# Performance work log

Measured on AMD Instinct MI355X. Metric: run time of the kernel, lower is better.

Reference implementation:

```python
import jax, jax.numpy as jnp
import numpy as np

N = 2048            # num nodes
AVG_DEG = 16
E0 = N * AVG_DEG    # random edges; self-loops appended -> E = E0 + N
IN_FEATS = 256
H = 16              # num_heads
HS = 32             # hidden_size (forced by linear001 = Linear(32,16))
D = HS // H         # head_dim = 2
EPS = 1e-5


def gat_conv(x, src, dst, W, al, ar, b):
    # DGL-style GATConv: x [N,F] -> [N,H,D]
    feat = (x @ W).reshape(N, H, D)                      # [N,H,D]
    el = (feat * al[None]).sum(-1)                       # [N,H] (src term)
    er = (feat * ar[None]).sum(-1)                       # [N,H] (dst term)
    e = jax.nn.leaky_relu(el[src] + er[dst], 0.2)        # [E,H]
    m = jax.ops.segment_max(e, dst, num_segments=N)      # segment softmax over incoming edges
    ex = jnp.exp(e - m[dst])
    s = jax.ops.segment_sum(ex, dst, num_segments=N)
    alpha = ex / s[dst]                                  # [E,H]
    out = jax.ops.segment_sum(alpha[:, :, None] * feat[src], dst, num_segments=N)
    return out + b.reshape(1, H, D)


def setup_inputs() -> dict:
    key = jax.random.key(0)
    ks = jax.random.split(key, 40)
    rn = lambda k, s, sc=0.1: (jax.random.normal(k, s, jnp.float32) * sc)
    loops = jnp.arange(N, dtype=jnp.int32)
    src = jnp.concatenate([jax.random.randint(ks[0], (E0,), 0, N, jnp.int32), loops])
    dst = jnp.concatenate([jax.random.randint(ks[1], (E0,), 0, N, jnp.int32), loops])
    inp = {
        'features': jax.random.normal(ks[2], (N, IN_FEATS), jnp.float32),
        'src': src, 'dst': dst,
        # GATConv 1
        'W1': rn(ks[3], (IN_FEATS, HS)), 'al1': rn(ks[4], (H, D)), 'ar1': rn(ks[5], (H, D)), 'bg1': rn(ks[6], (HS,)),
        # GATConv 2
        'W2': rn(ks[7], (HS, HS)), 'al2': rn(ks[8], (H, D)), 'ar2': rn(ks[9], (H, D)), 'bg2': rn(ks[10], (HS,)),
        # dense MHA projections
        'qw': rn(ks[11], (HS, HS)), 'qb': rn(ks[12], (HS,)),
        'kw': rn(ks[13], (HS, HS)), 'kb': rn(ks[14], (HS,)),
        'vw': rn(ks[15], (HS, HS)), 'vb': rn(ks[16], (HS,)),
        'ow': rn(ks[17], (HS, HS)), 'ob': rn(ks[18], (HS,)),
        # batchnorm affine
        'bn_g': jnp.ones((HS,), jnp.float32), 'bn_b': jnp.zeros((HS,), jnp.float32),
        # mlp
        'm1w': rn(ks[19], (HS, HS // 2)), 'm1b': rn(ks[20], (HS // 2,)),
        'm2w': rn(ks[21], (HS // 2, HS)), 'm2b': rn(ks[22], (HS,)),
        # scoring head
        'w001': rn(ks[23], (32, 16)), 'b001': rn(ks[24], (16,)),
        'w01': rn(ks[25], (16, 8)), 'b01': rn(ks[26], (8,)),
        'w1': rn(ks[27], (8, 4)), 'b1': rn(ks[28], (4,)),
        'w2': rn(ks[29], (4, 1)), 'b2': rn(ks[30], (1,)),
    }
    return inp


def reference(features, src, dst, W1, al1, ar1, bg1, W2, al2, ar2, bg2,
              qw, qb, kw, kb, vw, vb, ow, ob, bn_g, bn_b,
              m1w, m1b, m2w, m2b, w001, b001, w01, b01, w1, b1, w2, b2):
    h = gat_conv(features, src, dst, W1, al1, ar1, bg1).reshape(N, HS)
    h = gat_conv(h, src, dst, W2, al2, ar2, bg2).reshape(N, HS)
    # manual dense multi-head attention across all nodes
    Q = (h @ qw + qb).reshape(N, H, D)
    K = (h @ kw + kb).reshape(N, H, D)
    V = (h @ vw + vb).reshape(N, H, D)
    scores = jnp.einsum('nhd,mhd->hnm', Q, K) / jnp.sqrt(jnp.float32(D))  # [H,N,N]
    attn = jax.nn.softmax(scores, axis=-1)
    ao = jnp.einsum('hnm,mhd->nhd', attn, V).reshape(N, HS)
    ao = ao @ ow + ob
    # BatchNorm1d (training mode: batch stats, biased variance)
    mu = ao.mean(0)
    var = ao.var(0)
    ao = (ao - mu) / jnp.sqrt(var + EPS) * bn_g + bn_b
    # MLP
    ao = jax.nn.relu(ao @ m1w + m1b)
    ao = jax.nn.relu(ao @ m2w + m2b)
    # scoring head
    z = jax.nn.leaky_relu(ao @ w001 + b001, 0.01)
    z = jax.nn.leaky_relu(z @ w01 + b01, 0.01)
    z = jax.nn.leaky_relu(z @ w1 + b1, 0.01)
    return jax.nn.sigmoid(z @ w2 + b2)  # [N,1]
```

## Files before the change

### kernel.cpp

```cpp
#include <hip/hip_runtime.h>
#include <math.h>

#define NN 2048
#define NH 16
#define HSZ 32
#define INF_ 256

__global__ void k_gat1(const float* __restrict__ x, const float* __restrict__ W,
                       const float* __restrict__ al, const float* __restrict__ ar,
                       float* __restrict__ feat, float* __restrict__ el,
                       float* __restrict__ er, int* __restrict__ cnt,
                       int* __restrict__ cur, float* __restrict__ bnbuf) {
    __shared__ float xs[INF_];
    __shared__ float ps[256];
    __shared__ float fs[HSZ];
    int n = blockIdx.x, tid = threadIdx.x;
    xs[tid] = x[(size_t)n * INF_ + tid];
    if (tid == 0) cnt[n] = 0;
    if (tid == 1) cur[n] = 0;
    if (n == 0 && tid >= 128 && tid < 192) bnbuf[tid - 128] = 0.f;
    __syncthreads();
    int j = tid & 31, part = tid >> 5;
    float a = 0.f;
#pragma unroll
    for (int kk = 0; kk < 32; ++kk) {
        int k = part * 32 + kk;
        a += xs[k] * W[k * HSZ + j];
    }
    ps[tid] = a;
    __syncthreads();
    if (tid < HSZ) {
        float s = 0.f;
#pragma unroll
        for (int p = 0; p < 8; ++p) s += ps[p * 32 + tid];
        fs[tid] = s;
        feat[n * HSZ + tid] = s;
    }
    __syncthreads();
    if (tid < NH) {
        el[n * NH + tid] = fs[2 * tid] * al[2 * tid] + fs[2 * tid + 1] * al[2 * tid + 1];
    } else if (tid < 2 * NH) {
        int hh = tid - NH;
        er[n * NH + hh] = fs[2 * hh] * ar[2 * hh] + fs[2 * hh + 1] * ar[2 * hh + 1];
    }
}

__global__ void k_hist(int E, const int* __restrict__ dst, int* __restrict__ cnt) {
    int i = blockIdx.x * 256 + threadIdx.x;
    if (i < E) atomicAdd(&cnt[dst[i]], 1);
}

__global__ void k_scan(const int* __restrict__ cnt, int* __restrict__ off, int E) {
    __shared__ int ps[256];
    int t = threadIdx.x;
    int base = t * 8;
    int loc[8];
    int s = 0;
#pragma unroll
    for (int j = 0; j < 8; ++j) {
        loc[j] = s;
        s += cnt[base + j];
    }
    ps[t] = s;
    __syncthreads();
    for (int st = 1; st < 256; st <<= 1) {
        int v = (t >= st) ? ps[t - st] : 0;
        __syncthreads();
        ps[t] += v;
        __syncthreads();
    }
    int chunkbase = ps[t] - s;
#pragma unroll
    for (int j = 0; j < 8; ++j) off[base + j] = chunkbase + loc[j];
    if (t == 255) off[NN] = chunkbase + s;
}

__global__ void k_scatter(int E, const int* __restrict__ src, const int* __restrict__ dst,
                          const int* __restrict__ off, int* __restrict__ cur,
                          int* __restrict__ adj) {
    int i = blockIdx.x * 256 + threadIdx.x;
    if (i >= E) return;
    int d = dst[i];
    int p = atomicAdd(&cur[d], 1);
    adj[off[d] + p] = src[i];
}

__global__ void k_seg(const int* __restrict__ off, const int* __restrict__ adj,
                      const float* __restrict__ el, const float* __restrict__ er,
                      const float* __restrict__ feat, const float* __restrict__ bias,
                      float* __restrict__ hout) {
    int i = blockIdx.x * 256 + threadIdx.x;
    int n = i >> 4, h = i & 15;
    int o0 = off[n], o1 = off[n + 1];
    float erv = er[n * NH + h];
    float sum = 0.f, a0 = 0.f, a1 = 0.f;
    for (int j = o0; j < o1; ++j) {
        int s = adj[j];
        float v = el[s * NH + h] + erv;
        v = v > 0.f ? v : 0.2f * v;
        float ex = __expf(v);
        float2 f = ((const float2*)feat)[s * NH + h];
        sum += ex;
        a0 += ex * f.x;
        a1 += ex * f.y;
    }
    float rs = 1.f / sum;
    hout[n * HSZ + 2 * h] = a0 * rs + bias[2 * h];
    hout[n * HSZ + 2 * h + 1] = a1 * rs + bias[2 * h + 1];
}

__global__ void k_gat2(const float* __restrict__ h1, const float* __restrict__ W,
                       const float* __restrict__ al, const float* __restrict__ ar,
                       float* __restrict__ feat, float* __restrict__ el,
                       float* __restrict__ er) {
    __shared__ float hs[256];
    __shared__ float fs[256];
    int tid = threadIdx.x;
    int row0 = blockIdx.x * 8;
    int r = tid >> 5, j = tid & 31;
    hs[tid] = h1[row0 * HSZ + tid];
    __syncthreads();
    float a = 0.f;
#pragma unroll
    for (int c = 0; c < HSZ; ++c) a += hs[r * HSZ + c] * W[c * HSZ + j];
    fs[tid] = a;
    feat[row0 * HSZ + tid] = a;
    __syncthreads();
    if (tid < 128) {
        int rr = tid >> 4, hh = tid & 15;
        el[(row0 + rr) * NH + hh] =
            fs[rr * HSZ + 2 * hh] * al[2 * hh] + fs[rr * HSZ + 2 * hh + 1] * al[2 * hh + 1];
    } else {
        int t = tid - 128;
        int rr = t >> 4, hh = t & 15;
        er[(row0 + rr) * NH + hh] =
            fs[rr * HSZ + 2 * hh] * ar[2 * hh] + fs[rr * HSZ + 2 * hh + 1] * ar[2 * hh + 1];
    }
}

__global__ void k_qkv(const float* __restrict__ h2, const float* __restrict__ qw,
                      const float* __restrict__ qb, const float* __restrict__ kw,
                      const float* __restrict__ kb, const float* __restrict__ vw,
                      const float* __restrict__ vb, float* __restrict__ Q,
                      float* __restrict__ Kt, float* __restrict__ Vt) {
    __shared__ float hs[256];
    int tid = threadIdx.x;
    int row0 = blockIdx.x * 8;
    int r = tid >> 5, j = tid & 31;
    int n = row0 + r;
    hs[tid] = h2[row0 * HSZ + tid];
    __syncthreads();
    float q = qb[j], k = kb[j], v = vb[j];
#pragma unroll
    for (int c = 0; c < HSZ; ++c) {
        float hv = hs[r * HSZ + c];
        q += hv * qw[c * HSZ + j];
        k += hv * kw[c * HSZ + j];
        v += hv * vw[c * HSZ + j];
    }
    Q[n * HSZ + j] = q * 0.70710678118654752f;
    int hh = j >> 1, d = j & 1;
    Kt[hh * (NN * 2) + n * 2 + d] = k;
    Vt[hh * (NN * 2) + n * 2 + d] = v;
}

__global__ void k_attn(const float* __restrict__ Q, const float* __restrict__ Kt,
                       const float* __restrict__ Vt, float* __restrict__ ao) {
    int gtid = blockIdx.x * 256 + threadIdx.x;
    int wid = gtid >> 6;
    int lane = gtid & 63;
    int hh = wid >> 8;
    int q0 = (wid & 255) * 8;
    const float2* K2 = (const float2*)Kt + hh * NN;
    const float2* V2 = (const float2*)Vt + hh * NN;
    float qx[8], qy[8];
#pragma unroll
    for (int i = 0; i < 8; ++i) {
        float2 qq = ((const float2*)Q)[(q0 + i) * NH + hh];
        qx[i] = qq.x;
        qy[i] = qq.y;
    }
    float sm[8], a0[8], a1[8];
#pragma unroll
    for (int i = 0; i < 8; ++i) { sm[i] = 0.f; a0[i] = 0.f; a1[i] = 0.f; }
#pragma unroll 2
    for (int it = 0; it < NN / 64; ++it) {
        int mm = it * 64 + lane;
        float2 kk = K2[mm];
        float2 vv = V2[mm];
#pragma unroll
        for (int i = 0; i < 8; ++i) {
            float p = __expf(qx[i] * kk.x + qy[i] * kk.y);
            sm[i] += p;
            a0[i] += p * vv.x;
            a1[i] += p * vv.y;
        }
    }
#pragma unroll
    for (int i = 0; i < 8; ++i) {
#pragma unroll
        for (int off = 32; off > 0; off >>= 1) {
            sm[i] += __shfl_xor(sm[i], off);
            a0[i] += __shfl_xor(a0[i], off);
            a1[i] += __shfl_xor(a1[i], off);
        }
        if (lane == 0) {
            float rs = 1.f / sm[i];
            ((float2*)ao)[(q0 + i) * NH + hh] = make_float2(a0[i] * rs, a1[i] * rs);
        }
    }
}

__global__ void k_oproj(const float* __restrict__ ao, const float* __restrict__ ow,
                        const float* __restrict__ ob, float* __restrict__ X,
                        float* __restrict__ bnbuf) {
    __shared__ float as[256];
    __shared__ float xv[256];
    int tid = threadIdx.x;
    int row0 = blockIdx.x * 8;
    as[tid] = ao[row0 * HSZ + tid];
    __syncthreads();
    int r = tid >> 5, j = tid & 31;
    float a = ob[j];
#pragma unroll
    for (int c = 0; c < HSZ; ++c) a += as[r * HSZ + c] * ow[c * HSZ + j];
    X[(row0 + r) * HSZ + j] = a;
    xv[tid] = a;
    __syncthreads();
    if (tid < HSZ) {
        float s = 0.f, q = 0.f;
#pragma unroll
        for (int rr = 0; rr < 8; ++rr) {
            float v = xv[rr * HSZ + tid];
            s += v;
            q += v * v;
        }
        atomicAdd(&bnbuf[tid], s);
        atomicAdd(&bnbuf[HSZ + tid], q);
    }
}

__global__ void k_tail(const float* __restrict__ X, const float* __restrict__ bnbuf,
                       const float* __restrict__ bn_g, const float* __restrict__ bn_b,
                       const float* __restrict__ m1w, const float* __restrict__ m1b,
                       const float* __restrict__ m2w, const float* __restrict__ m2b,
                       const float* __restrict__ w001, const float* __restrict__ b001,
                       const float* __restrict__ w01, const float* __restrict__ b01,
                       const float* __restrict__ w1, const float* __restrict__ b1,
                       const float* __restrict__ w2, const float* __restrict__ b2,
                       float* __restrict__ out) {
    int n = blockIdx.x * 256 + threadIdx.x;
    const float invN = 1.f / NN;
    float x[HSZ];
#pragma unroll
    for (int i = 0; i < HSZ; ++i) {
        float mu = bnbuf[i] * invN;
        float var = bnbuf[HSZ + i] * invN - mu * mu;
        float rstd = rsqrtf(var + 1e-5f);
        x[i] = (X[n * HSZ + i] - mu) * rstd * bn_g[i] + bn_b[i];
    }
    float y[16];
#pragma unroll
    for (int j = 0; j < 16; ++j) {
        float a = m1b[j];
#pragma unroll
        for (int i = 0; i < HSZ; ++i) a += x[i] * m1w[i * 16 + j];
        y[j] = fmaxf(a, 0.f);
    }
    float z[HSZ];
#pragma unroll
    for (int j = 0; j < HSZ; ++j) {
        float a = m2b[j];
#pragma unroll
        for (int i = 0; i < 16; ++i) a += y[i] * m2w[i * HSZ + j];
        z[j] = fmaxf(a, 0.f);
    }
    float a16[16];
#pragma unroll
    for (int j = 0; j < 16; ++j) {
        float a = b001[j];
#pragma unroll
        for (int i = 0; i < HSZ; ++i) a += z[i] * w001[i * 16 + j];
        a16[j] = a > 0.f ? a : 0.01f * a;
    }
    float b8[8];
#pragma unroll
    for (int j = 0; j < 8; ++j) {
        float a = b01[j];
#pragma unroll
        for (int i = 0; i < 16; ++i) a += a16[i] * w01[i * 8 + j];
        b8[j] = a > 0.f ? a : 0.01f * a;
    }
    float c4[4];
#pragma unroll
    for (int j = 0; j < 4; ++j) {
        float a = b1[j];
#pragma unroll
        for (int i = 0; i < 8; ++i) a += b8[i] * w1[i * 4 + j];
        c4[j] = a > 0.f ? a : 0.01f * a;
    }
    float d = b2[0];
#pragma unroll
    for (int i = 0; i < 4; ++i) d += c4[i] * w2[i];
    out[n] = 1.f / (1.f + __expf(-d));
}

extern "C" void kernel_launch(void* const* d_in, const int* in_sizes, int n_in,
                              void* d_out, int out_size, void* d_ws, size_t ws_size,
                              hipStream_t stream) {
    const float* features = (const float*)d_in[0];
    const int* src = (const int*)d_in[1];
    const int* dst = (const int*)d_in[2];
    const float* W1 = (const float*)d_in[3];
    const float* al1 = (const float*)d_in[4];
    const float* ar1 = (const float*)d_in[5];
    const float* bg1 = (const float*)d_in[6];
    const float* W2 = (const float*)d_in[7];
    const float* al2 = (const float*)d_in[8];
    const float* ar2 = (const float*)d_in[9];
    const float* bg2 = (const float*)d_in[10];
    const float* qw = (const float*)d_in[11];
    const float* qb = (const float*)d_in[12];
    const float* kw = (const float*)d_in[13];
    const float* kb = (const float*)d_in[14];
    const float* vw = (const float*)d_in[15];
    const float* vb = (const float*)d_in[16];
    const float* ow = (const float*)d_in[17];
    const float* ob = (const float*)d_in[18];
    const float* bn_g = (const float*)d_in[19];
    const float* bn_b = (const float*)d_in[20];
    const float* m1w = (const float*)d_in[21];
    const float* m1b = (const float*)d_in[22];
    const float* m2w = (const float*)d_in[23];
    const float* m2b = (const float*)d_in[24];
    const float* w001 = (const float*)d_in[25];
    const float* b001 = (const float*)d_in[26];
    const float* w01 = (const float*)d_in[27];
    const float* b01 = (const float*)d_in[28];
    const float* w1 = (const float*)d_in[29];
    const float* b1 = (const float*)d_in[30];
    const float* w2 = (const float*)d_in[31];
    const float* b2 = (const float*)d_in[32];

    int E = in_sizes[1];

    float* ws = (float*)d_ws;
    float* feat = ws;
    float* el = feat + NN * HSZ;
    float* er = el + NN * NH;
    float* h1 = er + NN * NH;
    float* h2 = h1 + NN * HSZ;
    float* Q = h2 + NN * HSZ;
    float* Kt = Q + NN * HSZ;
    float* Vt = Kt + NN * HSZ;
    float* ao = Vt + NN * HSZ;
    float* X = ao + NN * HSZ;
    float* bnbuf = X + NN * HSZ;
    int* cnt = (int*)(bnbuf + 64);
    int* cur = cnt + NN;
    int* off = cur + NN;
    int* adj = off + NN + 1;

    dim3 b256(256);
    int gE = (E + 255) / 256;

    k_gat1<<<NN, b256, 0, stream>>>(features, W1, al1, ar1, feat, el, er, cnt, cur, bnbuf);
    k_hist<<<gE, b256, 0, stream>>>(E, dst, cnt);
    k_scan<<<1, b256, 0, stream>>>(cnt, off, E);
    k_scatter<<<gE, b256, 0, stream>>>(E, src, dst, off, cur, adj);
    k_seg<<<(NN * NH) / 256, b256, 0, stream>>>(off, adj, el, er, feat, bg1, h1);
    k_gat2<<<NN / 8, b256, 0, stream>>>(h1, W2, al2, ar2, feat, el, er);
    k_seg<<<(NN * NH) / 256, b256, 0, stream>>>(off, adj, el, er, feat, bg2, h2);
    k_qkv<<<NN / 8, b256, 0, stream>>>(h2, qw, qb, kw, kb, vw, vb, Q, Kt, Vt);
    k_attn<<<(NN * NH) / (8 * 4), b256, 0, stream>>>(Q, Kt, Vt, ao);
    k_oproj<<<NN / 8, b256, 0, stream>>>(ao, ow, ob, X, bnbuf);
    k_tail<<<NN / 256, b256, 0, stream>>>(X, bnbuf, bn_g, bn_b, m1w, m1b, m2w, m2b,
                                          w001, b001, w01, b01, w1, b1, w2, b2,
                                          (float*)d_out);
}
```

Baseline: 222.0 us.

## Fuse whole GAT+attention pipeline into one cooperative kernel with grid syncs

```diff
diff --git a/kernel.cpp b/kernel.cpp
--- a/kernel.cpp
+++ b/kernel.cpp
@@ -1,10 +1,286 @@
 #include <hip/hip_runtime.h>
+#include <hip/hip_cooperative_groups.h>
 #include <math.h>
+
+namespace cg = cooperative_groups;
 
 #define NN 2048
 #define NH 16
 #define HSZ 32
 #define INF_ 256
+#define NB 512
+#define NT 256
+#define CAP 64
+
+struct GParams {
+    const float *x, *W1, *al1, *ar1, *bg1;
+    const float *W2, *al2, *ar2, *bg2;
+    const float *qw, *qb, *kw, *kb, *vw, *vb, *ow, *ob;
+    const float *bn_g, *bn_b, *m1w, *m1b, *m2w, *m2b;
+    const float *w001, *b001, *w01, *b01, *w1, *b1, *w2, *b2;
+    const int *src, *dst;
+    float *feat, *el, *er, *feat2, *el2, *er2;
+    float *Q, *Kt, *Vt, *ao, *X, *bnbuf, *out;
+    int *cnt, *adj;
+    int E;
+};
+
+__launch_bounds__(NT, 2)
+__global__ void fused(GParams p) {
+    cg::grid_group grid = cg::this_grid();
+    __shared__ float xs[4][INF_];
+    __shared__ float row[4][HSZ];
+    __shared__ float xv[4][HSZ];
+    const int tid = threadIdx.x;
+    const int gtid = blockIdx.x * NT + tid;
+    const int lane = tid & 63;
+    const int wsl = tid >> 6;
+    const int gw = gtid >> 6;
+    const int j = lane & 31, half = lane >> 5;
+
+    for (int i = gtid; i < p.E; i += NB * NT) {
+        int d = p.dst[i];
+        int pos = atomicAdd(&p.cnt[d], 1);
+        if (pos < CAP) p.adj[d * CAP + pos] = p.src[i];
+    }
+    {
+        int n = gw;
+        ((float4*)xs[wsl])[lane] = ((const float4*)(p.x + (size_t)n * INF_))[lane];
+        __syncthreads();
+        float acc = 0.f;
+        const float4* x4 = (const float4*)xs[wsl];
+#pragma unroll
+        for (int k4 = 0; k4 < 32; ++k4) {
+            float4 xq = x4[half * 32 + k4];
+            int k = half * 128 + 4 * k4;
+            acc += xq.x * p.W1[(k + 0) * HSZ + j];
+            acc += xq.y * p.W1[(k + 1) * HSZ + j];
+            acc += xq.z * p.W1[(k + 2) * HSZ + j];
+            acc += xq.w * p.W1[(k + 3) * HSZ + j];
+        }
+        acc += __shfl_xor(acc, 32);
+        if (half == 0) {
+            p.feat[n * HSZ + j] = acc;
+            row[wsl][j] = acc;
+        }
+        __syncthreads();
+        if (lane < NH) {
+            p.el[n * NH + lane] =
+                row[wsl][2 * lane] * p.al1[2 * lane] + row[wsl][2 * lane + 1] * p.al1[2 * lane + 1];
+        } else if (lane < 2 * NH) {
+            int h = lane - NH;
+            p.er[n * NH + h] =
+                row[wsl][2 * h] * p.ar1[2 * h] + row[wsl][2 * h + 1] * p.ar1[2 * h + 1];
+        }
+    }
+    grid.sync();
+
+    {
+        int n = gw;
+        int h = lane >> 2, q = lane & 3;
+        int deg = p.cnt[n]; deg = deg < CAP ? deg : CAP;
+        int base = n * CAP;
+        float erv = p.er[n * NH + h];
+        float sum = 0.f, a0 = 0.f, a1 = 0.f;
+        for (int jj = q; jj < deg; jj += 4) {
+            int s = p.adj[base + jj];
+            float v = p.el[s * NH + h] + erv;
+            v = v > 0.f ? v : 0.2f * v;
+            float ex = __expf(v);
+            float2 f = ((const float2*)p.feat)[s * NH + h];
+            sum += ex; a0 += ex * f.x; a1 += ex * f.y;
+        }
+        sum += __shfl_xor(sum, 1); a0 += __shfl_xor(a0, 1); a1 += __shfl_xor(a1, 1);
+        sum += __shfl_xor(sum, 2); a0 += __shfl_xor(a0, 2); a1 += __shfl_xor(a1, 2);
+        if (q == 0) {
+            float rs = 1.f / sum;
+            row[wsl][2 * h]     = a0 * rs + p.bg1[2 * h];
+            row[wsl][2 * h + 1] = a1 * rs + p.bg1[2 * h + 1];
+        }
+        __syncthreads();
+        float acc = 0.f;
+#pragma unroll
+        for (int c = half * 16; c < half * 16 + 16; ++c) acc += row[wsl][c] * p.W2[c * HSZ + j];
+        acc += __shfl_xor(acc, 32);
+        if (half == 0) {
+            p.feat2[n * HSZ + j] = acc;
+            xv[wsl][j] = acc;
+        }
+        __syncthreads();
+        if (lane < NH) {
+            p.el2[n * NH + lane] =
+                xv[wsl][2 * lane] * p.al2[2 * lane] + xv[wsl][2 * lane + 1] * p.al2[2 * lane + 1];
+        } else if (lane < 2 * NH) {
+            int h2 = lane - NH;
+            p.er2[n * NH + h2] =
+                xv[wsl][2 * h2] * p.ar2[2 * h2] + xv[wsl][2 * h2 + 1] * p.ar2[2 * h2 + 1];
+        }
+    }
+    grid.sync();
+
+    {
+        int n = gw;
+        int h = lane >> 2, q = lane & 3;
+        int deg = p.cnt[n]; deg = deg < CAP ? deg : CAP;
+        int base = n * CAP;
+        float erv = p.er2[n * NH + h];
+        float sum = 0.f, a0 = 0.f, a1 = 0.f;
+        for (int jj = q; jj < deg; jj += 4) {
+            int s = p.adj[base + jj];
+            float v = p.el2[s * NH + h] + erv;
+            v = v > 0.f ? v : 0.2f * v;
+            float ex = __expf(v);
+            float2 f = ((const float2*)p.feat2)[s * NH + h];
+            sum += ex; a0 += ex * f.x; a1 += ex * f.y;
+        }
+        sum += __shfl_xor(sum, 1); a0 += __shfl_xor(a0, 1); a1 += __shfl_xor(a1, 1);
+        sum += __shfl_xor(sum, 2); a0 += __shfl_xor(a0, 2); a1 += __shfl_xor(a1, 2);
+        if (q == 0) {
+            float rs = 1.f / sum;
+            row[wsl][2 * h]     = a0 * rs + p.bg2[2 * h];
+            row[wsl][2 * h + 1] = a1 * rs + p.bg2[2 * h + 1];
+        }
+        __syncthreads();
+        float qa = 0.f, ka = 0.f, va = 0.f;
+#pragma unroll
+        for (int c = half * 16; c < half * 16 + 16; ++c) {
+            float hv = row[wsl][c];
+            qa += hv * p.qw[c * HSZ + j];
+            ka += hv * p.kw[c * HSZ + j];
+            va += hv * p.vw[c * HSZ + j];
+        }
+        qa += __shfl_xor(qa, 32);
+        ka += __shfl_xor(ka, 32);
+        va += __shfl_xor(va, 32);
+        if (half == 0) {
+            const float QS = 0.70710678118654752f * 1.44269504088896340f;
+            p.Q[n * HSZ + j] = (qa + p.qb[j]) * QS;
+            int hh = j >> 1, d = j & 1;
+            p.Kt[hh * (NN * 2) + n * 2 + d] = ka + p.kb[j];
+            p.Vt[hh * (NN * 2) + n * 2 + d] = va + p.vb[j];
+        }
+    }
+    grid.sync();
+
+    {
+        int hh = gw >> 7;
+        int q0 = (gw & 127) * 16;
+        const float2* K2 = (const float2*)p.Kt + hh * NN;
+        const float2* V2 = (const float2*)p.Vt + hh * NN;
+        float qx[16], qy[16], sm[16], a0[16], a1[16];
+#pragma unroll
+        for (int i = 0; i < 16; ++i) {
+            float2 qq = ((const float2*)p.Q)[(q0 + i) * NH + hh];
+            qx[i] = qq.x; qy[i] = qq.y;
+            sm[i] = 0.f; a0[i] = 0.f; a1[i] = 0.f;
+        }
+#pragma unroll 2
+        for (int it = 0; it < NN / 64; ++it) {
+            float2 kk = K2[it * 64 + lane];
+            float2 vv = V2[it * 64 + lane];
+#pragma unroll
+            for (int i = 0; i < 16; ++i) {
+                float pe = exp2f(qx[i] * kk.x + qy[i] * kk.y);
+                sm[i] += pe; a0[i] += pe * vv.x; a1[i] += pe * vv.y;
+            }
+        }
+#pragma unroll
+        for (int i = 0; i < 16; ++i) {
+#pragma unroll
+            for (int off = 32; off; off >>= 1) {
+                sm[i] += __shfl_xor(sm[i], off);
+                a0[i] += __shfl_xor(a0[i], off);
+                a1[i] += __shfl_xor(a1[i], off);
+            }
+            if (lane == 0) {
+                float rs = 1.f / sm[i];
+                ((float2*)p.ao)[(q0 + i) * NH + hh] = make_float2(a0[i] * rs, a1[i] * rs);
+            }
+        }
+    }
+    grid.sync();
+
+    {
+        int n = gw;
+        if (lane < HSZ) row[wsl][lane] = p.ao[n * HSZ + lane];
+        __syncthreads();
+        float acc = 0.f;
+#pragma unroll
+        for (int c = half * 16; c < half * 16 + 16; ++c) acc += row[wsl][c] * p.ow[c * HSZ + j];
+        acc += __shfl_xor(acc, 32);
+        if (half == 0) {
+            acc += p.ob[j];
+            p.X[n * HSZ + j] = acc;
+            xv[wsl][j] = acc;
+        }
+        __syncthreads();
+        if (tid < HSZ) {
+            float s = 0.f, qq = 0.f;
+#pragma unroll
+            for (int r = 0; r < 4; ++r) { float v = xv[r][tid]; s += v; qq += v * v; }
+            atomicAdd(&p.bnbuf[tid], s);
+            atomicAdd(&p.bnbuf[HSZ + tid], qq);
+        }
+    }
+    grid.sync();
+
+    if (gtid < NN) {
+        int n = gtid;
+        const float invN = 1.f / NN;
+        float xr[HSZ];
+#pragma unroll
+        for (int i = 0; i < HSZ; ++i) {
+            float mu = p.bnbuf[i] * invN;
+            float var = p.bnbuf[HSZ + i] * invN - mu * mu;
+            float rstd = rsqrtf(var + 1e-5f);
+            xr[i] = (p.X[n * HSZ + i] - mu) * rstd * p.bn_g[i] + p.bn_b[i];
+        }
+        float y[16];
+#pragma unroll
+        for (int jj = 0; jj < 16; ++jj) {
+            float a = p.m1b[jj];
+#pragma unroll
+            for (int i = 0; i < HSZ; ++i) a += xr[i] * p.m1w[i * 16 + jj];
+            y[jj] = fmaxf(a, 0.f);
+        }
+        float z[HSZ];
+#pragma unroll
+        for (int jj = 0; jj < HSZ; ++jj) {
+            float a = p.m2b[jj];
+#pragma unroll
+            for (int i = 0; i < 16; ++i) a += y[i] * p.m2w[i * HSZ + jj];
+            z[jj] = fmaxf(a, 0.f);
+        }
+        float a16[16];
+#pragma unroll
+        for (int jj = 0; jj < 16; ++jj) {
+            float a = p.b001[jj];
+#pragma unroll
+            for (int i = 0; i < HSZ; ++i) a += z[i] * p.w001[i * 16 + jj];
+            a16[jj] = a > 0.f ? a : 0.01f * a;
+        }
+        float b8[8];
+#pragma unroll
+        for (int jj = 0; jj < 8; ++jj) {
+            float a = p.b01[jj];
+#pragma unroll
+            for (int i = 0; i < 16; ++i) a += a16[i] * p.w01[i * 8 + jj];
+            b8[jj] = a > 0.f ? a : 0.01f * a;
+        }
+        float c4[4];
+#pragma unroll
+        for (int jj = 0; jj < 4; ++jj) {
+            float a = p.b1[jj];
+#pragma unroll
+            for (int i = 0; i < 8; ++i) a += b8[i] * p.w1[i * 4 + jj];
+            c4[jj] = a > 0.f ? a : 0.01f * a;
+        }
+        float d = p.b2[0];
+#pragma unroll
+        for (int i = 0; i < 4; ++i) d += c4[i] * p.w2[i];
+        p.out[n] = 1.f / (1.f + __expf(-d));
+    }
+}
 
 __global__ void k_gat1(const float* __restrict__ x, const float* __restrict__ W,
                        const float* __restrict__ al, const float* __restrict__ ar,
@@ -215,7 +491,7 @@
                         const float* __restrict__ ob, float* __restrict__ X,
                         float* __restrict__ bnbuf) {
     __shared__ float as[256];
-    __shared__ float xv[256];
+    __shared__ float xvv[256];
     int tid = threadIdx.x;
     int row0 = blockIdx.x * 8;
     as[tid] = ao[row0 * HSZ + tid];
@@ -225,13 +501,13 @@
 #pragma unroll
     for (int c = 0; c < HSZ; ++c) a += as[r * HSZ + c] * ow[c * HSZ + j];
     X[(row0 + r) * HSZ + j] = a;
-    xv[tid] = a;
+    xvv[tid] = a;
     __syncthreads();
     if (tid < HSZ) {
         float s = 0.f, q = 0.f;
 #pragma unroll
         for (int rr = 0; rr < 8; ++rr) {
-            float v = xv[rr * HSZ + tid];
+            float v = xvv[rr * HSZ + tid];
             s += v;
             q += v * v;
         }
@@ -344,11 +620,14 @@
 
     int E = in_sizes[1];
 
-    float* ws = (float*)d_ws;
-    float* feat = ws;
+    float* wsp = (float*)d_ws;
+    float* feat = wsp;
     float* el = feat + NN * HSZ;
     float* er = el + NN * NH;
-    float* h1 = er + NN * NH;
+    float* feat2 = er + NN * NH;
+    float* el2 = feat2 + NN * HSZ;
+    float* er2 = el2 + NN * NH;
+    float* h1 = er2 + NN * NH;
     float* h2 = h1 + NN * HSZ;
     float* Q = h2 + NN * HSZ;
     float* Kt = Q + NN * HSZ;
@@ -361,20 +640,40 @@
     int* off = cur + NN;
     int* adj = off + NN + 1;
 
-    dim3 b256(256);
-    int gE = (E + 255) / 256;
-
-    k_gat1<<<NN, b256, 0, stream>>>(features, W1, al1, ar1, feat, el, er, cnt, cur, bnbuf);
-    k_hist<<<gE, b256, 0, stream>>>(E, dst, cnt);
-    k_scan<<<1, b256, 0, stream>>>(cnt, off, E);
-    k_scatter<<<gE, b256, 0, stream>>>(E, src, dst, off, cur, adj);
-    k_seg<<<(NN * NH) / 256, b256, 0, stream>>>(off, adj, el, er, feat, bg1, h1);
-    k_gat2<<<NN / 8, b256, 0, stream>>>(h1, W2, al2, ar2, feat, el, er);
-    k_seg<<<(NN * NH) / 256, b256, 0, stream>>>(off, adj, el, er, feat, bg2, h2);
-    k_qkv<<<NN / 8, b256, 0, stream>>>(h2, qw, qb, kw, kb, vw, vb, Q, Kt, Vt);
-    k_attn<<<(NN * NH) / (8 * 4), b256, 0, stream>>>(Q, Kt, Vt, ao);
-    k_oproj<<<NN / 8, b256, 0, stream>>>(ao, ow, ob, X, bnbuf);
-    k_tail<<<NN / 256, b256, 0, stream>>>(X, bnbuf, bn_g, bn_b, m1w, m1b, m2w, m2b,
-                                          w001, b001, w01, b01, w1, b1, w2, b2,
-                                          (float*)d_out);
-}
+    hipMemsetAsync(bnbuf, 0, (64 + NN) * sizeof(float), stream);
+
+    GParams pr;
+    pr.x = features; pr.W1 = W1; pr.al1 = al1; pr.ar1 = ar1; pr.bg1 = bg1;
+    pr.W2 = W2; pr.al2 = al2; pr.ar2 = ar2; pr.bg2 = bg2;
+    pr.qw = qw; pr.qb = qb; pr.kw = kw; pr.kb = kb; pr.vw = vw; pr.vb = vb;
+    pr.ow = ow; pr.ob = ob; pr.bn_g = bn_g; pr.bn_b = bn_b;
+    pr.m1w = m1w; pr.m1b = m1b; pr.m2w = m2w; pr.m2b = m2b;
+    pr.w001 = w001; pr.b001 = b001; pr.w01 = w01; pr.b01 = b01;
+    pr.w1 = w1; pr.b1 = b1; pr.w2 = w2; pr.b2 = b2;
+    pr.src = src; pr.dst = dst;
+    pr.feat = feat; pr.el = el; pr.er = er; pr.feat2 = feat2; pr.el2 = el2; pr.er2 = er2;
+    pr.Q = Q; pr.Kt = Kt; pr.Vt = Vt; pr.ao = ao; pr.X = X; pr.bnbuf = bnbuf;
+    pr.out = (float*)d_out;
+    pr.cnt = cnt; pr.adj = adj; pr.E = E;
+
+    void* args[] = { &pr };
+    hipError_t err = hipLaunchCooperativeKernel((const void*)fused, dim3(NB), dim3(NT),
+                                                args, 0, stream);
+    if (err != hipSuccess) {
+        dim3 b256(256);
+        int gE = (E + 255) / 256;
+        k_gat1<<<NN, b256, 0, stream>>>(features, W1, al1, ar1, feat, el, er, cnt, cur, bnbuf);
+        k_hist<<<gE, b256, 0, stream>>>(E, dst, cnt);
+        k_scan<<<1, b256, 0, stream>>>(cnt, off, E);
+        k_scatter<<<gE, b256, 0, stream>>>(E, src, dst, off, cur, adj);
+        k_seg<<<(NN * NH) / 256, b256, 0, stream>>>(off, adj, el, er, feat, bg1, h1);
+        k_gat2<<<NN / 8, b256, 0, stream>>>(h1, W2, al2, ar2, feat, el, er);
+        k_seg<<<(NN * NH) / 256, b256, 0, stream>>>(off, adj, el, er, feat, bg2, h2);
+        k_qkv<<<NN / 8, b256, 0, stream>>>(h2, qw, qb, kw, kb, vw, vb, Q, Kt, Vt);
+        k_attn<<<(NN * NH) / (8 * 4), b256, 0, stream>>>(Q, Kt, Vt, ao);
+        k_oproj<<<NN / 8, b256, 0, stream>>>(ao, ow, ob, X, bnbuf);
+        k_tail<<<NN / 256, b256, 0, stream>>>(X, bnbuf, bn_g, bn_b, m1w, m1b, m2w, m2b,
+                                              w001, b001, w01, b01, w1, b1, w2, b2,
+                                              (float*)d_out);
+    }
+}
```

New measurement: 498.2 us. 124% more time.
